# Optimization experiments

Measured on AMD Instinct MI355X. Metric: run time of the kernel, lower is better.

The kernel has to match this reference:

```python
import jax, jax.numpy as jnp
import numpy as np

HIDDEN = 512
HEADS = 8
HEAD_DIM = HIDDEN // HEADS


def setup_inputs() -> dict:
    key = jax.random.key(0)
    ks = jax.random.split(key, 9)
    B, S = 4, 2048
    scale = 1.0 / np.sqrt(HIDDEN)
    x = jax.random.normal(ks[0], (B, S, HIDDEN), dtype=jnp.float32)
    Wq = jax.random.normal(ks[1], (HIDDEN, HIDDEN), dtype=jnp.float32) * scale
    Wk = jax.random.normal(ks[2], (HIDDEN, HIDDEN), dtype=jnp.float32) * scale
    Wv = jax.random.normal(ks[3], (HIDDEN, HIDDEN), dtype=jnp.float32) * scale
    Wo = jax.random.normal(ks[4], (HIDDEN, HIDDEN), dtype=jnp.float32) * scale
    bq = jax.random.normal(ks[5], (HIDDEN,), dtype=jnp.float32) * 0.01
    bk = jax.random.normal(ks[6], (HIDDEN,), dtype=jnp.float32) * 0.01
    bv = jax.random.normal(ks[7], (HIDDEN,), dtype=jnp.float32) * 0.01
    bo = jax.random.normal(ks[8], (HIDDEN,), dtype=jnp.float32) * 0.01
    return {"x": x, "Wq": Wq, "bq": bq, "Wk": Wk, "bk": bk,
            "Wv": Wv, "bv": bv, "Wo": Wo, "bo": bo}


def reference(x, Wq, bq, Wk, bk, Wv, bv, Wo, bo):
    B, S, _ = x.shape
    # project and split heads: [B, H, S, D]
    def split_heads(t):
        return t.reshape(B, S, HEADS, HEAD_DIM).transpose(0, 2, 1, 3)
    Q = split_heads(x @ Wq.T + bq)
    K = split_heads(x @ Wk.T + bk)
    V = split_heads(x @ Wv.T + bv)
    scores = jnp.einsum("bhsd,bhtd->bhst", Q, K) / jnp.sqrt(
        jnp.array(HEAD_DIM, dtype=x.dtype))
    attn = jax.nn.softmax(scores, axis=-1)  # dropout is identity in eval
    ctx = jnp.einsum("bhst,bhtd->bhsd", attn, V)
    ctx = ctx.transpose(0, 2, 1, 3).reshape(B, S, HIDDEN)
    return ctx @ Wo.T + bo
```

## Files before the change

kernel.cpp:

```cpp
#include <hip/hip_runtime.h>
#include <stdint.h>

#define HID 512
#define NH 8
#define HD 64
#define BB 4
#define SS 2048

typedef unsigned short u16;
typedef __attribute__((ext_vector_type(8))) short short8;
typedef __attribute__((ext_vector_type(4))) float f32x4;
typedef __attribute__((ext_vector_type(4))) _Float16 f16x4;
typedef __attribute__((ext_vector_type(2))) unsigned int uint2v;

#define MFMA16(a, b, c) __builtin_amdgcn_mfma_f32_16x16x32_bf16((a), (b), (c), 0, 0, 0)
#define MFMAH16(a, b, c) __builtin_amdgcn_mfma_f32_16x16x16f16((a), (b), (c), 0, 0, 0)

#define WAIT_VM4() __builtin_amdgcn_s_waitcnt(0xF74)
#define WAIT_VM3() __builtin_amdgcn_s_waitcnt(0xF73)
#define WAIT_VM0() __builtin_amdgcn_s_waitcnt(0xF70)
#define PIPE_BARRIER() do { asm volatile("" ::: "memory"); \
  __builtin_amdgcn_s_barrier(); asm volatile("" ::: "memory"); } while (0)

__device__ __forceinline__ u16 f2bf(float f) {
  union { float f; uint32_t u; } v; v.f = f;
  return (u16)((v.u + 0x7fffu + ((v.u >> 16) & 1u)) >> 16);
}

__device__ __forceinline__ u16 f2h(float f) {
  _Float16 h = (_Float16)f;
  return __builtin_bit_cast(u16, h);
}

__device__ __forceinline__ void gl_lds16(const u16* g, u16* l) {
  __builtin_amdgcn_global_load_lds(
      (const __attribute__((address_space(1))) unsigned int*)g,
      (__attribute__((address_space(3))) unsigned int*)l, 16, 0, 0);
}

__global__ void prep(const float* __restrict__ x,
                     const float* __restrict__ w0, const float* __restrict__ w1,
                     const float* __restrict__ w2, const float* __restrict__ w3,
                     u16* __restrict__ xb,
                     u16* __restrict__ o0, u16* __restrict__ o1,
                     u16* __restrict__ o2, u16* __restrict__ o3) {
  const int bid = blockIdx.x;
  const float* in;
  u16* out;
  int base;
  if (bid < 2048) {
    in = x; out = xb; base = bid * 2048;
  } else {
    const int z = (bid - 2048) >> 7;
    base = ((bid - 2048) & 127) * 2048;
    in = (z == 0) ? w0 : (z == 1) ? w1 : (z == 2) ? w2 : w3;
    out = (z == 0) ? o0 : (z == 1) ? o1 : (z == 2) ? o2 : o3;
  }
  const int i = base + threadIdx.x * 8;
  float4 v0 = *(const float4*)(in + i);
  float4 v1 = *(const float4*)(in + i + 4);
  ushort4 a, b;
  a.x = f2bf(v0.x); a.y = f2bf(v0.y); a.z = f2bf(v0.z); a.w = f2bf(v0.w);
  b.x = f2bf(v1.x); b.y = f2bf(v1.y); b.z = f2bf(v1.z); b.w = f2bf(v1.w);
  *(ushort4*)(out + i) = a;
  *(ushort4*)(out + i + 4) = b;
}

__global__ __launch_bounds__(256, 3)
void qkv_gemm(const u16* __restrict__ xb,
              const u16* __restrict__ wq, const u16* __restrict__ wk, const u16* __restrict__ wv,
              const float* __restrict__ bq, const float* __restrict__ bk, const float* __restrict__ bv,
              u16* __restrict__ Q, u16* __restrict__ K, u16* __restrict__ Vt) {
  __shared__ u16 sA[3][4096];
  __shared__ u16 sB[3][4096];
  const int tid = threadIdx.x;
  const int lane = tid & 63;
  const int wave = tid >> 6;
  const int l15 = lane & 15;
  const int quad = lane >> 4;
  const int wm = wave >> 1, wn = wave & 1;

  const int L = blockIdx.x;
  const int xcd = L & 7;
  const int slot = L >> 3;
  const int bm = xcd * 8 + (slot & 7);
  const int r2 = slot >> 3;
  const int bn = r2 & 3;
  const int z = r2 >> 2;

  const float* bias = (z == 0) ? bq : (z == 1) ? bk : bv;
  const float scale = (z == 0) ? 0.18033688011112042f : 1.0f;

  const u16* Arows = (z == 2) ? wv : xb;
  const u16* Brows = (z == 2) ? xb : ((z == 0) ? wq : wk);
  const int am0 = (z == 2) ? (bn * 128) : (bm * 128);
  const int bn0 = (z == 2) ? (bm * 128) : (bn * 128);

  const int srow = tid >> 2;
  const int sg = (tid & 3) ^ ((srow >> 1) & 3);
  const u16* gA = Arows + (am0 + srow) * 512 + sg * 8;
  const u16* gB = Brows + (bn0 + srow) * 512 + sg * 8;

  const int fsw = (quad ^ ((l15 >> 1) & 3)) * 8;
  int aoff[4], boff[4];
#pragma unroll
  for (int t = 0; t < 4; ++t) {
    aoff[t] = (wm * 64 + t * 16 + l15) * 32 + fsw;
    boff[t] = (wn * 64 + t * 16 + l15) * 32 + fsw;
  }

  f32x4 acc[4][4] = {};

#pragma unroll
  for (int t = 0; t < 2; ++t) {
    const int k0 = t * 32;
    gl_lds16(gA + k0, &sA[t][wave * 512]);
    gl_lds16(gA + k0 + 64 * 512, &sA[t][2048 + wave * 512]);
    gl_lds16(gB + k0, &sB[t][wave * 512]);
    gl_lds16(gB + k0 + 64 * 512, &sB[t][2048 + wave * 512]);
  }

  for (int kk = 0; kk < 16; ++kk) {
    WAIT_VM4();
    PIPE_BARRIER();
    {
      const int tp = (kk + 2 < 16) ? kk + 2 : 15;
      const int ns = (kk + 2) % 3;
      const int k0 = tp * 32;
      gl_lds16(gA + k0, &sA[ns][wave * 512]);
      gl_lds16(gA + k0 + 64 * 512, &sA[ns][2048 + wave * 512]);
      gl_lds16(gB + k0, &sB[ns][wave * 512]);
      gl_lds16(gB + k0 + 64 * 512, &sB[ns][2048 + wave * 512]);
    }
    const int cur = kk % 3;
    short8 af[4], bf[4];
#pragma unroll
    for (int t = 0; t < 4; ++t) af[t] = *(const short8*)&sA[cur][aoff[t]];
#pragma unroll
    for (int t = 0; t < 4; ++t) bf[t] = *(const short8*)&sB[cur][boff[t]];
#pragma unroll
    for (int mi = 0; mi < 4; ++mi)
#pragma unroll
      for (int ni = 0; ni < 4; ++ni)
        acc[mi][ni] = MFMA16(af[mi], bf[ni], acc[mi][ni]);
  }

  if (z != 2) {
    u16* dst = (z == 0) ? Q : K;
#pragma unroll
    for (int mi = 0; mi < 4; ++mi) {
#pragma unroll
      for (int ni = 0; ni < 4; ++ni) {
        const int col = bn0 + wn * 64 + ni * 16 + l15;
        const float bs = bias[col];
#pragma unroll
        for (int i = 0; i < 4; ++i) {
          const int row = am0 + wm * 64 + mi * 16 + quad * 4 + i;
          const float v = (acc[mi][ni][i] + bs) * scale;
          const int b = row >> 11, s = row & 2047;
          const int h = col >> 6, d = col & 63;
          dst[(((size_t)(b * 8 + h) * 2048 + s) << 6) + d] = f2bf(v);
        }
      }
    }
  } else {
#pragma unroll
    for (int mi = 0; mi < 4; ++mi) {
#pragma unroll
      for (int i = 0; i < 4; ++i) {
        const int o = am0 + wm * 64 + mi * 16 + quad * 4 + i;
        const float bs = bias[o];
        const int h = o >> 6, d = o & 63;
#pragma unroll
        for (int ni = 0; ni < 4; ++ni) {
          const int r = bn0 + wn * 64 + ni * 16 + l15;
          const int b = r >> 11, s = r & 2047;
          Vt[(((size_t)(b * 8 + h) * 64 + d) << 11) + s] = f2h(acc[mi][ni][i] + bs);
        }
      }
    }
  }
}

__global__ __launch_bounds__(512, 4)
void attn(const u16* __restrict__ Q, const u16* __restrict__ K,
          const u16* __restrict__ Vt, u16* __restrict__ ctx) {
  __shared__ __align__(16) u16 smem[4 * 8192];
  const int tid = threadIdx.x;
  const int lane = tid & 63;
  const int wave = tid >> 6;
  const int l15 = lane & 15;
  const int quad = lane >> 4;
  const int pair = wave >> 1;
  const int par = wave & 1;

  const int L = blockIdx.x;
  const int xcd = L & 7;
  const int slotb = L >> 3;
  const int bh = xcd * 4 + (slotb & 3);
  const int qt = slotb >> 2;

  const u16* Qb = Q + (size_t)bh * SS * HD;
  const u16* Kb = K + (size_t)bh * SS * HD;
  const u16* Vb = Vt + (size_t)bh * HD * SS;

  const int rowbase = qt * 128 + pair * 32;
  short8 qf[2][2];
#pragma unroll
  for (int rf = 0; rf < 2; ++rf)
#pragma unroll
    for (int kc = 0; kc < 2; ++kc)
      qf[rf][kc] = *(const short8*)(Qb + (rowbase + rf * 16 + l15) * 64 + kc * 32 + quad * 8);
  asm volatile("" ::: "memory");

  f32x4 oacc[2][4] = {};
  float plsum[2] = {0.f, 0.f};

  const int trow = tid >> 3;
  const int gsw = (tid & 7) ^ (trow & 7);
  const int kOff = trow * 64 + gsw * 8;
  const int vOff = trow * 2048 + gsw * 8;
  u16* ldsK = smem + tid * 8;
  u16* ldsV = smem + 4096 + tid * 8;

  const int l7 = l15 & 7;
  int kfo[2];
#pragma unroll
  for (int kc = 0; kc < 2; ++kc)
    kfo[kc] = (par * 32 + l15) * 64 + ((kc * 4 + quad) ^ l7) * 8;
  int vfo[2];
#pragma unroll
  for (int tb = 0; tb < 2; ++tb)
    vfo[tb] = l15 * 64 + (((par * 4 + tb * 2 + (quad >> 1)) ^ l7) * 8) + (quad & 1) * 4;

#pragma unroll
  for (int t = 0; t < 3; ++t) {
    gl_lds16(Kb + t * 4096 + kOff, ldsK + t * 8192);
    gl_lds16(Vb + t * 64 + vOff, ldsV + t * 8192);
  }

  for (int tt = 0; tt < 32; ++tt) {
    WAIT_VM4();
    PIPE_BARRIER();
    {
      const int tp = (tt + 3 < 32) ? tt + 3 : 31;
      const int ns = (tt + 3) & 3;
      gl_lds16(Kb + tp * 4096 + kOff, ldsK + ns * 8192);
      gl_lds16(Vb + tp * 64 + vOff, ldsV + ns * 8192);
    }
    const int cb = (tt & 3) * 8192;

#pragma unroll
    for (int tb = 0; tb < 2; ++tb) {
      const short8 k0 = *(const short8*)&smem[cb + tb * 1024 + kfo[0]];
      const short8 k1 = *(const short8*)&smem[cb + tb * 1024 + kfo[1]];
      f32x4 sacc[2] = {};
      __builtin_amdgcn_s_setprio(1);
#pragma unroll
      for (int rf = 0; rf < 2; ++rf) {
        sacc[rf] = MFMA16(k0, qf[rf][0], sacc[rf]);
        sacc[rf] = MFMA16(k1, qf[rf][1], sacc[rf]);
      }
      __builtin_amdgcn_s_setprio(0);
      uint2v vf[4];
#pragma unroll
      for (int nd = 0; nd < 4; ++nd)
        vf[nd] = *(const uint2v*)&smem[cb + 4096 + nd * 1024 + vfo[tb]];
#pragma unroll
      for (int rf = 0; rf < 2; ++rf) {
        const float p0 = __builtin_amdgcn_exp2f(sacc[rf][0]);
        const float p1 = __builtin_amdgcn_exp2f(sacc[rf][1]);
        const float p2 = __builtin_amdgcn_exp2f(sacc[rf][2]);
        const float p3 = __builtin_amdgcn_exp2f(sacc[rf][3]);
        plsum[rf] += (p0 + p1) + (p2 + p3);
        uint2v pu;
        pu.x = __builtin_bit_cast(unsigned int, __builtin_amdgcn_cvt_pkrtz(p0, p1));
        pu.y = __builtin_bit_cast(unsigned int, __builtin_amdgcn_cvt_pkrtz(p2, p3));
        const f16x4 pf = __builtin_bit_cast(f16x4, pu);
        __builtin_amdgcn_s_setprio(1);
#pragma unroll
        for (int nd = 0; nd < 4; ++nd)
          oacc[rf][nd] = MFMAH16(pf, __builtin_bit_cast(f16x4, vf[nd]), oacc[rf][nd]);
        __builtin_amdgcn_s_setprio(0);
      }
    }
  }

  WAIT_VM0();
  __syncthreads();

#pragma unroll
  for (int rf = 0; rf < 2; ++rf) {
    plsum[rf] += __shfl_xor(plsum[rf], 16);
    plsum[rf] += __shfl_xor(plsum[rf], 32);
  }

  float* cbuf = (float*)smem;
  float* lbuf = cbuf + 128 * 68;
  if (par) {
#pragma unroll
    for (int rf = 0; rf < 2; ++rf) {
#pragma unroll
      for (int nd = 0; nd < 4; ++nd)
#pragma unroll
        for (int i = 0; i < 4; ++i)
          cbuf[(pair * 32 + rf * 16 + quad * 4 + i) * 68 + nd * 16 + l15] = oacc[rf][nd][i];
      if (quad == 0) lbuf[pair * 32 + rf * 16 + l15] = plsum[rf];
    }
  }
  __syncthreads();
  if (!par) {
    const int b = bh >> 3, h = bh & 7;
#pragma unroll
    for (int rf = 0; rf < 2; ++rf) {
      const float tot = plsum[rf] + lbuf[pair * 32 + rf * 16 + l15];
      float inv[4];
#pragma unroll
      for (int i = 0; i < 4; ++i)
        inv[i] = __builtin_amdgcn_rcpf(__shfl(tot, quad * 4 + i));
#pragma unroll
      for (int nd = 0; nd < 4; ++nd)
#pragma unroll
        for (int i = 0; i < 4; ++i) {
          const float v = (oacc[rf][nd][i] +
                           cbuf[(pair * 32 + rf * 16 + quad * 4 + i) * 68 + nd * 16 + l15]) * inv[i];
          const int s = rowbase + rf * 16 + quad * 4 + i;
          const int d = nd * 16 + l15;
          ctx[((size_t)(b * 2048 + s) << 9) + h * 64 + d] = f2bf(v);
        }
    }
  }
}

__global__ __launch_bounds__(256, 2)
void out_gemm(const u16* __restrict__ A, const u16* __restrict__ W,
              const float* __restrict__ bias, float* __restrict__ out) {
  __shared__ u16 sA[3][4096];
  __shared__ u16 sB[3][2048];
  const int tid = threadIdx.x;
  const int lane = tid & 63;
  const int wave = tid >> 6;
  const int l15 = lane & 15;
  const int quad = lane >> 4;

  const int L = blockIdx.x;
  const int xcd = L & 7;
  const int slot = L >> 3;
  const int bm = xcd * 8 + (slot & 7);
  const int bn = slot >> 3;

  const int srow = tid >> 2;
  const int sg = (tid & 3) ^ ((srow >> 1) & 3);
  const u16* gA = A + (bm * 128 + srow) * 512 + sg * 8;
  const u16* gB = W + (bn * 64 + srow) * 512 + sg * 8;

  const int fsw = (quad ^ ((l15 >> 1) & 3)) * 8;
  int aoff[2], boff[4];
#pragma unroll
  for (int t = 0; t < 2; ++t) aoff[t] = (wave * 32 + t * 16 + l15) * 32 + fsw;
#pragma unroll
  for (int t = 0; t < 4; ++t) boff[t] = (t * 16 + l15) * 32 + fsw;

  f32x4 acc[2][4] = {};

#pragma unroll
  for (int t = 0; t < 2; ++t) {
    const int k0 = t * 32;
    gl_lds16(gA + k0, &sA[t][wave * 512]);
    gl_lds16(gA + k0 + 64 * 512, &sA[t][2048 + wave * 512]);
    gl_lds16(gB + k0, &sB[t][wave * 512]);
  }

  for (int kk = 0; kk < 16; ++kk) {
    WAIT_VM3();
    PIPE_BARRIER();
    {
      const int tp = (kk + 2 < 16) ? kk + 2 : 15;
      const int ns = (kk + 2) % 3;
      const int k0 = tp * 32;
      gl_lds16(gA + k0, &sA[ns][wave * 512]);
      gl_lds16(gA + k0 + 64 * 512, &sA[ns][2048 + wave * 512]);
      gl_lds16(gB + k0, &sB[ns][wave * 512]);
    }
    const int cur = kk % 3;
    short8 af[2], bf[4];
#pragma unroll
    for (int t = 0; t < 2; ++t) af[t] = *(const short8*)&sA[cur][aoff[t]];
#pragma unroll
    for (int t = 0; t < 4; ++t) bf[t] = *(const short8*)&sB[cur][boff[t]];
#pragma unroll
    for (int mi = 0; mi < 2; ++mi)
#pragma unroll
      for (int ni = 0; ni < 4; ++ni)
        acc[mi][ni] = MFMA16(af[mi], bf[ni], acc[mi][ni]);
  }

#pragma unroll
  for (int mi = 0; mi < 2; ++mi) {
#pragma unroll
    for (int ni = 0; ni < 4; ++ni) {
      const int col = bn * 64 + ni * 16 + l15;
      const float bs = bias[col];
#pragma unroll
      for (int i = 0; i < 4; ++i) {
        const int row = bm * 128 + wave * 32 + mi * 16 + quad * 4 + i;
        out[(size_t)row * 512 + col] = acc[mi][ni][i] + bs;
      }
    }
  }
}

extern "C" void kernel_launch(void* const* d_in, const int* in_sizes, int n_in,
                              void* d_out, int out_size, void* d_ws, size_t ws_size,
                              hipStream_t stream) {
  const float* x = (const float*)d_in[0];
  const float* Wq = (const float*)d_in[1];
  const float* bq = (const float*)d_in[2];
  const float* Wk = (const float*)d_in[3];
  const float* bk = (const float*)d_in[4];
  const float* Wv = (const float*)d_in[5];
  const float* bv = (const float*)d_in[6];
  const float* Wo = (const float*)d_in[7];
  const float* bo = (const float*)d_in[8];
  float* out = (float*)d_out;

  char* ws = (char*)d_ws;
  u16* xb  = (u16*)(ws);
  u16* wqb = (u16*)(ws + (8u << 20));
  u16* wkb = (u16*)(ws + (8u << 20) + (512u << 10));
  u16* wvb = (u16*)(ws + (9u << 20));
  u16* wob = (u16*)(ws + (9u << 20) + (512u << 10));
  u16* Qb  = (u16*)(ws + (10u << 20));
  u16* Kb  = (u16*)(ws + (18u << 20));
  u16* Vtb = (u16*)(ws + (26u << 20));
  u16* ctx = (u16*)(ws + (34u << 20));

  prep<<<2560, 256, 0, stream>>>(x, Wq, Wk, Wv, Wo, xb, wqb, wkb, wvb, wob);
  qkv_gemm<<<768, 256, 0, stream>>>(xb, wqb, wkb, wvb, bq, bk, bv, Qb, Kb, Vtb);
  attn<<<512, 512, 0, stream>>>(Qb, Kb, Vtb, ctx);
  out_gemm<<<512, 256, 0, stream>>>(ctx, wob, bo, out);
}
```

Baseline: 154.8 us.

## Double-buffer attention KV tiles in pairs and shrink out-projection tiles to 64x64

The attention loop now loads two KV tiles per step into a double buffer. It waits for all outstanding loads once per pair of tiles, which halves the number of barriers compared with the previous 4-stage ring that waited per tile. The output GEMM moves from 128x64 to 64x64 tiles with 1024 blocks and a launch bound of 4 blocks per CU. This raises occupancy and parallelism at the cost of less A/B reuse per block. The WAIT_VM0 in attention also exposes full load latency at each pair boundary, which may reduce overlap.

```diff
diff --git a/kernel.cpp b/kernel.cpp
--- a/kernel.cpp
+++ b/kernel.cpp
@@ -18,6 +18,7 @@
 
 #define WAIT_VM4() __builtin_amdgcn_s_waitcnt(0xF74)
 #define WAIT_VM3() __builtin_amdgcn_s_waitcnt(0xF73)
+#define WAIT_VM2() __builtin_amdgcn_s_waitcnt(0xF72)
 #define WAIT_VM0() __builtin_amdgcn_s_waitcnt(0xF70)
 #define PIPE_BARRIER() do { asm volatile("" ::: "memory"); \
   __builtin_amdgcn_s_barrier(); asm volatile("" ::: "memory"); } while (0)
@@ -234,54 +235,59 @@
     vfo[tb] = l15 * 64 + (((par * 4 + tb * 2 + (quad >> 1)) ^ l7) * 8) + (quad & 1) * 4;
 
 #pragma unroll
-  for (int t = 0; t < 3; ++t) {
-    gl_lds16(Kb + t * 4096 + kOff, ldsK + t * 8192);
-    gl_lds16(Vb + t * 64 + vOff, ldsV + t * 8192);
-  }
-
-  for (int tt = 0; tt < 32; ++tt) {
-    WAIT_VM4();
+  for (int tp = 0; tp < 2; ++tp) {
+    gl_lds16(Kb + tp * 4096 + kOff, ldsK + tp * 8192);
+    gl_lds16(Vb + tp * 64 + vOff, ldsV + tp * 8192);
+  }
+
+  for (int u = 0; u < 16; ++u) {
+    WAIT_VM0();
     PIPE_BARRIER();
-    {
-      const int tp = (tt + 3 < 32) ? tt + 3 : 31;
-      const int ns = (tt + 3) & 3;
-      gl_lds16(Kb + tp * 4096 + kOff, ldsK + ns * 8192);
-      gl_lds16(Vb + tp * 64 + vOff, ldsV + ns * 8192);
-    }
-    const int cb = (tt & 3) * 8192;
-
-#pragma unroll
-    for (int tb = 0; tb < 2; ++tb) {
-      const short8 k0 = *(const short8*)&smem[cb + tb * 1024 + kfo[0]];
-      const short8 k1 = *(const short8*)&smem[cb + tb * 1024 + kfo[1]];
-      f32x4 sacc[2] = {};
-      __builtin_amdgcn_s_setprio(1);
-#pragma unroll
-      for (int rf = 0; rf < 2; ++rf) {
-        sacc[rf] = MFMA16(k0, qf[rf][0], sacc[rf]);
-        sacc[rf] = MFMA16(k1, qf[rf][1], sacc[rf]);
+    if (u < 15) {
+      const int ns = (u + 1) & 1;
+#pragma unroll
+      for (int tp = 0; tp < 2; ++tp) {
+        const int T = (u + 1) * 2 + tp;
+        gl_lds16(Kb + T * 4096 + kOff, ldsK + ns * 16384 + tp * 8192);
+        gl_lds16(Vb + T * 64 + vOff, ldsV + ns * 16384 + tp * 8192);
       }
-      __builtin_amdgcn_s_setprio(0);
-      uint2v vf[4];
-#pragma unroll
-      for (int nd = 0; nd < 4; ++nd)
-        vf[nd] = *(const uint2v*)&smem[cb + 4096 + nd * 1024 + vfo[tb]];
-#pragma unroll
-      for (int rf = 0; rf < 2; ++rf) {
-        const float p0 = __builtin_amdgcn_exp2f(sacc[rf][0]);
-        const float p1 = __builtin_amdgcn_exp2f(sacc[rf][1]);
-        const float p2 = __builtin_amdgcn_exp2f(sacc[rf][2]);
-        const float p3 = __builtin_amdgcn_exp2f(sacc[rf][3]);
-        plsum[rf] += (p0 + p1) + (p2 + p3);
-        uint2v pu;
-        pu.x = __builtin_bit_cast(unsigned int, __builtin_amdgcn_cvt_pkrtz(p0, p1));
-        pu.y = __builtin_bit_cast(unsigned int, __builtin_amdgcn_cvt_pkrtz(p2, p3));
-        const f16x4 pf = __builtin_bit_cast(f16x4, pu);
+    }
+#pragma unroll
+    for (int tp = 0; tp < 2; ++tp) {
+      const int cb = (u & 1) * 16384 + tp * 8192;
+#pragma unroll
+      for (int tb = 0; tb < 2; ++tb) {
+        const short8 k0 = *(const short8*)&smem[cb + tb * 1024 + kfo[0]];
+        const short8 k1 = *(const short8*)&smem[cb + tb * 1024 + kfo[1]];
+        f32x4 sacc[2] = {};
         __builtin_amdgcn_s_setprio(1);
 #pragma unroll
+        for (int rf = 0; rf < 2; ++rf) {
+          sacc[rf] = MFMA16(k0, qf[rf][0], sacc[rf]);
+          sacc[rf] = MFMA16(k1, qf[rf][1], sacc[rf]);
+        }
+        __builtin_amdgcn_s_setprio(0);
+        uint2v vf[4];
+#pragma unroll
         for (int nd = 0; nd < 4; ++nd)
-          oacc[rf][nd] = MFMAH16(pf, __builtin_bit_cast(f16x4, vf[nd]), oacc[rf][nd]);
-        __builtin_amdgcn_s_setprio(0);
+          vf[nd] = *(const uint2v*)&smem[cb + 4096 + nd * 1024 + vfo[tb]];
+#pragma unroll
+        for (int rf = 0; rf < 2; ++rf) {
+          const float p0 = __builtin_amdgcn_exp2f(sacc[rf][0]);
+          const float p1 = __builtin_amdgcn_exp2f(sacc[rf][1]);
+          const float p2 = __builtin_amdgcn_exp2f(sacc[rf][2]);
+          const float p3 = __builtin_amdgcn_exp2f(sacc[rf][3]);
+          plsum[rf] += (p0 + p1) + (p2 + p3);
+          uint2v pu;
+          pu.x = __builtin_bit_cast(unsigned int, __builtin_amdgcn_cvt_pkrtz(p0, p1));
+          pu.y = __builtin_bit_cast(unsigned int, __builtin_amdgcn_cvt_pkrtz(p2, p3));
+          const f16x4 pf = __builtin_bit_cast(f16x4, pu);
+          __builtin_amdgcn_s_setprio(1);
+#pragma unroll
+          for (int nd = 0; nd < 4; ++nd)
+            oacc[rf][nd] = MFMAH16(pf, __builtin_bit_cast(f16x4, vf[nd]), oacc[rf][nd]);
+          __builtin_amdgcn_s_setprio(0);
+        }
       }
     }
   }
@@ -332,10 +338,10 @@
   }
 }
 
-__global__ __launch_bounds__(256, 2)
+__global__ __launch_bounds__(256, 4)
 void out_gemm(const u16* __restrict__ A, const u16* __restrict__ W,
               const float* __restrict__ bias, float* __restrict__ out) {
-  __shared__ u16 sA[3][4096];
+  __shared__ u16 sA[3][2048];
   __shared__ u16 sB[3][2048];
   const int tid = threadIdx.x;
   const int lane = tid & 63;
@@ -346,66 +352,57 @@
   const int L = blockIdx.x;
   const int xcd = L & 7;
   const int slot = L >> 3;
-  const int bm = xcd * 8 + (slot & 7);
-  const int bn = slot >> 3;
+  const int bm = xcd * 16 + (slot & 15);
+  const int bn = slot >> 4;
 
   const int srow = tid >> 2;
   const int sg = (tid & 3) ^ ((srow >> 1) & 3);
-  const u16* gA = A + (bm * 128 + srow) * 512 + sg * 8;
+  const u16* gA = A + (bm * 64 + srow) * 512 + sg * 8;
   const u16* gB = W + (bn * 64 + srow) * 512 + sg * 8;
 
   const int fsw = (quad ^ ((l15 >> 1) & 3)) * 8;
-  int aoff[2], boff[4];
-#pragma unroll
-  for (int t = 0; t < 2; ++t) aoff[t] = (wave * 32 + t * 16 + l15) * 32 + fsw;
+  const int aoff = (wave * 16 + l15) * 32 + fsw;
+  int boff[4];
 #pragma unroll
   for (int t = 0; t < 4; ++t) boff[t] = (t * 16 + l15) * 32 + fsw;
 
-  f32x4 acc[2][4] = {};
+  f32x4 acc[4] = {};
 
 #pragma unroll
   for (int t = 0; t < 2; ++t) {
     const int k0 = t * 32;
     gl_lds16(gA + k0, &sA[t][wave * 512]);
-    gl_lds16(gA + k0 + 64 * 512, &sA[t][2048 + wave * 512]);
     gl_lds16(gB + k0, &sB[t][wave * 512]);
   }
 
   for (int kk = 0; kk < 16; ++kk) {
-    WAIT_VM3();
+    WAIT_VM2();
     PIPE_BARRIER();
     {
       const int tp = (kk + 2 < 16) ? kk + 2 : 15;
       const int ns = (kk + 2) % 3;
       const int k0 = tp * 32;
       gl_lds16(gA + k0, &sA[ns][wave * 512]);
-      gl_lds16(gA + k0 + 64 * 512, &sA[ns][2048 + wave * 512]);
       gl_lds16(gB + k0, &sB[ns][wave * 512]);
     }
     const int cur = kk % 3;
-    short8 af[2], bf[4];
-#pragma unroll
-    for (int t = 0; t < 2; ++t) af[t] = *(const short8*)&sA[cur][aoff[t]];
+    short8 af, bf[4];
+    af = *(const short8*)&sA[cur][aoff];
 #pragma unroll
     for (int t = 0; t < 4; ++t) bf[t] = *(const short8*)&sB[cur][boff[t]];
 #pragma unroll
-    for (int mi = 0; mi < 2; ++mi)
-#pragma unroll
-      for (int ni = 0; ni < 4; ++ni)
-        acc[mi][ni] = MFMA16(af[mi], bf[ni], acc[mi][ni]);
-  }
-
-#pragma unroll
-  for (int mi = 0; mi < 2; ++mi) {
-#pragma unroll
-    for (int ni = 0; ni < 4; ++ni) {
-      const int col = bn * 64 + ni * 16 + l15;
-      const float bs = bias[col];
-#pragma unroll
-      for (int i = 0; i < 4; ++i) {
-        const int row = bm * 128 + wave * 32 + mi * 16 + quad * 4 + i;
-        out[(size_t)row * 512 + col] = acc[mi][ni][i] + bs;
-      }
+    for (int ni = 0; ni < 4; ++ni)
+      acc[ni] = MFMA16(af, bf[ni], acc[ni]);
+  }
+
+#pragma unroll
+  for (int ni = 0; ni < 4; ++ni) {
+    const int col = bn * 64 + ni * 16 + l15;
+    const float bs = bias[col];
+#pragma unroll
+    for (int i = 0; i < 4; ++i) {
+      const int row = bm * 64 + wave * 16 + quad * 4 + i;
+      out[(size_t)row * 512 + col] = acc[ni][i] + bs;
     }
   }
 }
@@ -438,5 +435,5 @@
   prep<<<2560, 256, 0, stream>>>(x, Wq, Wk, Wv, Wo, xb, wqb, wkb, wvb, wob);
   qkv_gemm<<<768, 256, 0, stream>>>(xb, wqb, wkb, wvb, bq, bk, bv, Qb, Kb, Vtb);
   attn<<<512, 512, 0, stream>>>(Qb, Kb, Vtb, ctx);
-  out_gemm<<<512, 256, 0, stream>>>(ctx, wob, bo, out);
-}
+  out_gemm<<<1024, 256, 0, stream>>>(ctx, wob, bo, out);
+}
```

New measurement: 163.9 us. 1.06x slower.

## Use 16x16x32 f16 MFMA for PV with reshuffled K row mapping

Applied to the files above, without the earlier changes.

Replaces the two 16x16x16 f16 MFMAs per tile block in the P·V product with a single 16x16x32 f16 MFMA over a 32-key slice. K rows are permuted across the two score sub-blocks so that the eight exp values each lane produces line up with the 8-wide f16 operand layout, and the K global-to-LDS swizzle changes to match. V fragments are read as 128-bit LDS loads instead of 64-bit loads. This halves the PV MFMA instruction count and the number of LDS reads, at the cost of more live registers per iteration and a trickier swizzle that must stay consistent between writers and readers.

```diff
diff --git a/kernel.cpp b/kernel.cpp
--- a/kernel.cpp
+++ b/kernel.cpp
@@ -11,10 +11,12 @@
 typedef __attribute__((ext_vector_type(8))) short short8;
 typedef __attribute__((ext_vector_type(4))) float f32x4;
 typedef __attribute__((ext_vector_type(4))) _Float16 f16x4;
+typedef __attribute__((ext_vector_type(8))) _Float16 f16x8;
 typedef __attribute__((ext_vector_type(2))) unsigned int uint2v;
+typedef __attribute__((ext_vector_type(4))) unsigned int uint4v;
 
 #define MFMA16(a, b, c) __builtin_amdgcn_mfma_f32_16x16x32_bf16((a), (b), (c), 0, 0, 0)
-#define MFMAH16(a, b, c) __builtin_amdgcn_mfma_f32_16x16x16f16((a), (b), (c), 0, 0, 0)
+#define MFMAH32(a, b, c) __builtin_amdgcn_mfma_f32_16x16x32_f16((a), (b), (c), 0, 0, 0)
 
 #define WAIT_VM4() __builtin_amdgcn_s_waitcnt(0xF74)
 #define WAIT_VM3() __builtin_amdgcn_s_waitcnt(0xF73)
@@ -217,21 +219,23 @@
   float plsum[2] = {0.f, 0.f};
 
   const int trow = tid >> 3;
-  const int gsw = (tid & 7) ^ (trow & 7);
-  const int kOff = trow * 64 + gsw * 8;
-  const int vOff = trow * 2048 + gsw * 8;
+  const int rK = (trow & 3) | (((trow >> 3) & 1) << 2);
+  const int gswK = (tid & 7) ^ rK;
+  const int gswV = (tid & 7) ^ (trow & 7);
+  const int kOff = trow * 64 + gswK * 8;
+  const int vOff = trow * 2048 + gswV * 8;
   u16* ldsK = smem + tid * 8;
   u16* ldsV = smem + 4096 + tid * 8;
 
   const int l7 = l15 & 7;
-  int kfo[2];
-#pragma unroll
-  for (int kc = 0; kc < 2; ++kc)
-    kfo[kc] = (par * 32 + l15) * 64 + ((kc * 4 + quad) ^ l7) * 8;
-  int vfo[2];
-#pragma unroll
-  for (int tb = 0; tb < 2; ++tb)
-    vfo[tb] = l15 * 64 + (((par * 4 + tb * 2 + (quad >> 1)) ^ l7) * 8) + (quad & 1) * 4;
+  const int tKbase = par * 32 + ((l15 >> 2) * 8) + (l15 & 3);
+  int kfo[2][2];
+#pragma unroll
+  for (int s = 0; s < 2; ++s)
+#pragma unroll
+    for (int kc = 0; kc < 2; ++kc)
+      kfo[s][kc] = (tKbase + 4 * s) * 64 + (((kc * 4 + quad) ^ l7) * 8);
+  const int vfoV = l15 * 64 + (((par * 4 + quad) ^ l7) * 8);
 
 #pragma unroll
   for (int t = 0; t < 3; ++t) {
@@ -250,39 +254,48 @@
     }
     const int cb = (tt & 3) * 8192;
 
-#pragma unroll
-    for (int tb = 0; tb < 2; ++tb) {
-      const short8 k0 = *(const short8*)&smem[cb + tb * 1024 + kfo[0]];
-      const short8 k1 = *(const short8*)&smem[cb + tb * 1024 + kfo[1]];
-      f32x4 sacc[2] = {};
+    short8 ks[2][2];
+#pragma unroll
+    for (int s = 0; s < 2; ++s)
+#pragma unroll
+      for (int kc = 0; kc < 2; ++kc)
+        ks[s][kc] = *(const short8*)&smem[cb + kfo[s][kc]];
+    f32x4 sacc[2][2] = {};
+    __builtin_amdgcn_s_setprio(1);
+#pragma unroll
+    for (int s = 0; s < 2; ++s)
+#pragma unroll
+      for (int rf = 0; rf < 2; ++rf) {
+        sacc[s][rf] = MFMA16(ks[s][0], qf[rf][0], sacc[s][rf]);
+        sacc[s][rf] = MFMA16(ks[s][1], qf[rf][1], sacc[s][rf]);
+      }
+    __builtin_amdgcn_s_setprio(0);
+    short8 vraw[4];
+#pragma unroll
+    for (int nd = 0; nd < 4; ++nd)
+      vraw[nd] = *(const short8*)&smem[cb + 4096 + nd * 1024 + vfoV];
+#pragma unroll
+    for (int rf = 0; rf < 2; ++rf) {
+      const float p0 = __builtin_amdgcn_exp2f(sacc[0][rf][0]);
+      const float p1 = __builtin_amdgcn_exp2f(sacc[0][rf][1]);
+      const float p2 = __builtin_amdgcn_exp2f(sacc[0][rf][2]);
+      const float p3 = __builtin_amdgcn_exp2f(sacc[0][rf][3]);
+      const float p4 = __builtin_amdgcn_exp2f(sacc[1][rf][0]);
+      const float p5 = __builtin_amdgcn_exp2f(sacc[1][rf][1]);
+      const float p6 = __builtin_amdgcn_exp2f(sacc[1][rf][2]);
+      const float p7 = __builtin_amdgcn_exp2f(sacc[1][rf][3]);
+      plsum[rf] += ((p0 + p1) + (p2 + p3)) + ((p4 + p5) + (p6 + p7));
+      uint4v pw;
+      pw.x = __builtin_bit_cast(unsigned int, __builtin_amdgcn_cvt_pkrtz(p0, p1));
+      pw.y = __builtin_bit_cast(unsigned int, __builtin_amdgcn_cvt_pkrtz(p2, p3));
+      pw.z = __builtin_bit_cast(unsigned int, __builtin_amdgcn_cvt_pkrtz(p4, p5));
+      pw.w = __builtin_bit_cast(unsigned int, __builtin_amdgcn_cvt_pkrtz(p6, p7));
+      const f16x8 pf = __builtin_bit_cast(f16x8, pw);
       __builtin_amdgcn_s_setprio(1);
 #pragma unroll
-      for (int rf = 0; rf < 2; ++rf) {
-        sacc[rf] = MFMA16(k0, qf[rf][0], sacc[rf]);
-        sacc[rf] = MFMA16(k1, qf[rf][1], sacc[rf]);
-      }
+      for (int nd = 0; nd < 4; ++nd)
+        oacc[rf][nd] = MFMAH32(pf, __builtin_bit_cast(f16x8, vraw[nd]), oacc[rf][nd]);
       __builtin_amdgcn_s_setprio(0);
-      uint2v vf[4];
-#pragma unroll
-      for (int nd = 0; nd < 4; ++nd)
-        vf[nd] = *(const uint2v*)&smem[cb + 4096 + nd * 1024 + vfo[tb]];
-#pragma unroll
-      for (int rf = 0; rf < 2; ++rf) {
-        const float p0 = __builtin_amdgcn_exp2f(sacc[rf][0]);
-        const float p1 = __builtin_amdgcn_exp2f(sacc[rf][1]);
-        const float p2 = __builtin_amdgcn_exp2f(sacc[rf][2]);
-        const float p3 = __builtin_amdgcn_exp2f(sacc[rf][3]);
-        plsum[rf] += (p0 + p1) + (p2 + p3);
-        uint2v pu;
-        pu.x = __builtin_bit_cast(unsigned int, __builtin_amdgcn_cvt_pkrtz(p0, p1));
-        pu.y = __builtin_bit_cast(unsigned int, __builtin_amdgcn_cvt_pkrtz(p2, p3));
-        const f16x4 pf = __builtin_bit_cast(f16x4, pu);
-        __builtin_amdgcn_s_setprio(1);
-#pragma unroll
-        for (int nd = 0; nd < 4; ++nd)
-          oacc[rf][nd] = MFMAH16(pf, __builtin_bit_cast(f16x4, vf[nd]), oacc[rf][nd]);
-        __builtin_amdgcn_s_setprio(0);
-      }
     }
   }
 
```

Result: no change. 156.1 us (+0.9%).
